# Performance work log

Measured on AMD Instinct MI355X. Metric: run time of the kernel, lower is better.

Reference implementation:

```python
import jax, jax.numpy as jnp
import numpy as np

KS = 3
ST = 1


def _windows(x, ks, st):
    """im2col sliding windows: (bs, c, h, w) -> (bs, c, H', W', ks, ks)
    where windows[b,c,i,j,k,f] = x[b,c, i*st+k, j*st+f] (matches torch as_strided)."""
    bs, c, h, w = x.shape
    Hp = (h - ks) // st + 1
    Wp = (w - ks) // st + 1
    return jnp.stack(
        [jnp.stack([x[:, :, k:k + Hp * st:st, f:f + Wp * st:st] for f in range(ks)], axis=-1)
         for k in range(ks)], axis=-2)


def setup_inputs() -> dict:
    key = jax.random.key(0)
    k1, k2, k3 = jax.random.split(key, 3)
    x = jax.random.normal(k1, (16, 16, 64, 512), dtype=jnp.float32)
    points = jax.random.normal(k2, (16, 3, 64, 512), dtype=jnp.float32)
    kernel = jax.random.normal(k3, (32, 16, 4), dtype=jnp.float32) * 0.05
    return {"x": x, "kernel": kernel, "points": points}


def reference(x, kernel, points):
    ks, st = KS, ST
    # (bs, in_c, H', W', ks, ks) overlapping patches of features and xyz coords
    strided_x = _windows(x, ks, st)
    strided_pts = _windows(points, ks, st)
    bd = ks // 2 if st == 1 else ks // 4
    # center point of each window: (bs, 3, H', W')
    ctr = points[:, :, bd:-bd, bd:-bd][:, :, ::st, ::st]
    # point-relative coordinates per window element: (bs, 3, H', W', ks, ks)
    rel_pts = ctr[..., None, None] - strided_pts
    # homogeneous coordinate -> d = 4
    rel_pts = jnp.concatenate([rel_pts, jnp.ones_like(rel_pts[:, :1])], axis=1)
    # kernel: (out_c, in_c, 4)
    return jnp.einsum('bdhwkf,bihwkf,oid->bohw', rel_pts, strided_x, kernel)
```

## Files before the change

kernel.cpp:

```cpp
#include <hip/hip_runtime.h>
#include <hip/hip_bf16.h>


#define HH 64
#define WW 512
#define HP 62
#define WP 510
#define IC 16
#define OC 32
#define BS 16
#define RB 2
#define TR (RB + 2)
#define TC 64
#define LC 68
#define NPL 19
#define CPR 17
#define NROWS (NPL * TR)
#define NCHUNK (NROWS * CPR)

typedef __attribute__((ext_vector_type(8))) short short8;
typedef __attribute__((ext_vector_type(4))) float f32x4;

static __device__ __forceinline__ short f2bf(float f) {
    union { __hip_bfloat16 h; short s; } u;
    u.h = __float2bfloat16(f);
    return u.s;
}

__global__ __launch_bounds__(256) void flex_conv_async(
    const float* __restrict__ x, const float* __restrict__ kern,
    const float* __restrict__ pts, float* __restrict__ out)
{
    __shared__ float lds[NPL * TR * LC];

    const int tid = threadIdx.x;
    const int j0 = blockIdx.x * TC;
    const int i0 = blockIdx.y * RB;
    const int b = blockIdx.z;

    const float* xb = x + (size_t)b * IC * HH * WW;
    const float* pb = pts + (size_t)b * 3 * HH * WW;

    #pragma unroll
    for (int rnd = 0; rnd < 6; ++rnd) {
        const int cid = tid + rnd * 256;
        if (cid < NCHUNK) {
            const int row = cid / CPR;
            const int chunk = cid - row * CPR;
            const int plane = row >> 2;
            const int rr = row & (TR - 1);
            const float* base = (plane < IC)
                ? (xb + (size_t)plane * HH * WW)
                : (pb + (size_t)(plane - IC) * HH * WW);
            int gcol = j0 + chunk * 4;
            if (gcol > WW - 4) gcol = WW - 4;
            const float* g = base + (size_t)(i0 + rr) * WW + gcol;
            __builtin_amdgcn_global_load_lds(
                (const __attribute__((address_space(1))) void*)g,
                (__attribute__((address_space(3))) void*)(lds + (size_t)cid * 4),
                16, 0, 0);
        }
    }

    const int lane = tid & 63;
    const int wave = tid >> 6;
    const int p = lane & 15;
    const int c = lane >> 4;
    const int tc = wave * 16 + p;

    short8 a0lo, a0hi, a1lo, a1hi;
    {
        const float4* k0v = (const float4*)(kern + (size_t)p * 64 + c * 8);
        const float4* k1v = (const float4*)(kern + (size_t)(16 + p) * 64 + c * 8);
        float4 v0a = k0v[0], v0b = k0v[1], v0c = k0v[8], v0d = k0v[9];
        float4 v1a = k1v[0], v1b = k1v[1], v1c = k1v[8], v1d = k1v[9];
        a0lo[0]=f2bf(v0a.x); a0lo[1]=f2bf(v0a.y); a0lo[2]=f2bf(v0a.z); a0lo[3]=f2bf(v0a.w);
        a0lo[4]=f2bf(v0b.x); a0lo[5]=f2bf(v0b.y); a0lo[6]=f2bf(v0b.z); a0lo[7]=f2bf(v0b.w);
        a0hi[0]=f2bf(v0c.x); a0hi[1]=f2bf(v0c.y); a0hi[2]=f2bf(v0c.z); a0hi[3]=f2bf(v0c.w);
        a0hi[4]=f2bf(v0d.x); a0hi[5]=f2bf(v0d.y); a0hi[6]=f2bf(v0d.z); a0hi[7]=f2bf(v0d.w);
        a1lo[0]=f2bf(v1a.x); a1lo[1]=f2bf(v1a.y); a1lo[2]=f2bf(v1a.z); a1lo[3]=f2bf(v1a.w);
        a1lo[4]=f2bf(v1b.x); a1lo[5]=f2bf(v1b.y); a1lo[6]=f2bf(v1b.z); a1lo[7]=f2bf(v1b.w);
        a1hi[0]=f2bf(v1c.x); a1hi[1]=f2bf(v1c.y); a1hi[2]=f2bf(v1c.z); a1hi[3]=f2bf(v1c.w);
        a1hi[4]=f2bf(v1d.x); a1hi[5]=f2bf(v1d.y); a1hi[6]=f2bf(v1d.z); a1hi[7]=f2bf(v1d.w);
    }

    __syncthreads();

    float xs[4][RB], px0[4][RB], px1[4][RB], px2[4][RB];
    #pragma unroll
    for (int t = 0; t < 4; ++t)
        #pragma unroll
        for (int q = 0; q < RB; ++q) { xs[t][q]=0.f; px0[t][q]=0.f; px1[t][q]=0.f; px2[t][q]=0.f; }
    float c0v[RB], c1v[RB], c2v[RB];

    #pragma unroll
    for (int rr = 0; rr < TR; ++rr) {
        const float* lp0 = &lds[(IC * TR + rr) * LC + tc];
        const float* lp1 = &lds[((IC + 1) * TR + rr) * LC + tc];
        const float* lp2 = &lds[((IC + 2) * TR + rr) * LC + tc];
        const float pa0 = lp0[0], pm0 = lp0[1], pz0 = lp0[2];
        const float pa1 = lp1[0], pm1 = lp1[1], pz1 = lp1[2];
        const float pa2 = lp2[0], pm2 = lp2[1], pz2 = lp2[2];
        if (rr >= 1 && rr <= RB) { c0v[rr-1] = pm0; c1v[rr-1] = pm1; c2v[rr-1] = pm2; }
        #pragma unroll
        for (int t = 0; t < 4; ++t) {
            const int ic = (t >> 1) * 8 + 2 * c + (t & 1);
            const float* lx = &lds[(ic * TR + rr) * LC + tc];
            const float x0 = lx[0], x1 = lx[1], x2 = lx[2];
            const float rsx = x0 + x1 + x2;
            float r0 = pa0 * x0; r0 = fmaf(pm0, x1, r0); r0 = fmaf(pz0, x2, r0);
            float r1 = pa1 * x0; r1 = fmaf(pm1, x1, r1); r1 = fmaf(pz1, x2, r1);
            float r2 = pa2 * x0; r2 = fmaf(pm2, x1, r2); r2 = fmaf(pz2, x2, r2);
            #pragma unroll
            for (int q = 0; q < RB; ++q) {
                if (rr >= q && rr <= q + 2) {
                    xs[t][q] += rsx; px0[t][q] += r0; px1[t][q] += r1; px2[t][q] += r2;
                }
            }
        }
    }

    const int j = j0 + tc;
    #pragma unroll
    for (int q = 0; q < RB; ++q) {
        short8 blo, bhi;
        #pragma unroll
        for (int t = 0; t < 4; ++t) {
            const short t0 = f2bf(fmaf(c0v[q], xs[t][q], -px0[t][q]));
            const short t1 = f2bf(fmaf(c1v[q], xs[t][q], -px1[t][q]));
            const short t2 = f2bf(fmaf(c2v[q], xs[t][q], -px2[t][q]));
            const short t3 = f2bf(xs[t][q]);
            const int s = (t & 1) * 4;
            if (t < 2) { blo[s+0]=t0; blo[s+1]=t1; blo[s+2]=t2; blo[s+3]=t3; }
            else       { bhi[s+0]=t0; bhi[s+1]=t1; bhi[s+2]=t2; bhi[s+3]=t3; }
        }
        f32x4 acc0 = {0.f,0.f,0.f,0.f}, acc1 = {0.f,0.f,0.f,0.f};
        acc0 = __builtin_amdgcn_mfma_f32_16x16x32_bf16(a0lo, blo, acc0, 0, 0, 0);
        acc0 = __builtin_amdgcn_mfma_f32_16x16x32_bf16(a0hi, bhi, acc0, 0, 0, 0);
        acc1 = __builtin_amdgcn_mfma_f32_16x16x32_bf16(a1lo, blo, acc1, 0, 0, 0);
        acc1 = __builtin_amdgcn_mfma_f32_16x16x32_bf16(a1hi, bhi, acc1, 0, 0, 0);
        if (j < WP) {
            float* ob = out + (size_t)b * OC * HP * WP + (size_t)(i0 + q) * WP + j;
            #pragma unroll
            for (int r = 0; r < 4; ++r) {
                const int o = c * 4 + r;
                ob[(size_t)o * HP * WP]        = acc0[r];
                ob[(size_t)(o + 16) * HP * WP] = acc1[r];
            }
        }
    }
}

extern "C" void kernel_launch(void* const* d_in, const int* in_sizes, int n_in,
                              void* d_out, int out_size, void* d_ws, size_t ws_size,
                              hipStream_t stream)
{
    const float* x    = (const float*)d_in[0];
    const float* kern = (const float*)d_in[1];
    const float* pts  = (const float*)d_in[2];
    float* out = (float*)d_out;

    dim3 block(256, 1, 1);
    dim3 grid(WW / TC, HP / RB, BS);
    flex_conv_async<<<grid, block, 0, stream>>>(x, kern, pts, out);
}
```

Measured before the change: 118.4 us.

## Double-buffer LDS tiles across a persistent row loop with taller row blocks

Each block now walks four consecutive row tiles and double-buffers the LDS staging. The next tile's global-to-LDS async loads are issued before computing the current one, so memory latency overlaps with compute. The row block grows from 2 to 4 output rows, which cuts the redundant halo rows loaded per output row. The cost is a much smaller grid (512 blocks instead of several thousand), about 62KB of LDS per block, and clamped duplicate work on the last tile. All of this can reduce occupancy and latency hiding.

After: 115.4 us. 2.6% less time.

```diff
diff --git a/kernel.cpp b/kernel.cpp
--- a/kernel.cpp
+++ b/kernel.cpp
@@ -9,7 +9,7 @@
 #define IC 16
 #define OC 32
 #define BS 16
-#define RB 2
+#define RB 4
 #define TR (RB + 2)
 #define TC 64
 #define LC 68
@@ -17,6 +17,9 @@
 #define CPR 17
 #define NROWS (NPL * TR)
 #define NCHUNK (NROWS * CPR)
+#define NRND 8
+#define TPG 4
+#define LDSZ (NPL * TR * LC)
 
 typedef __attribute__((ext_vector_type(8))) short short8;
 typedef __attribute__((ext_vector_type(4))) float f32x4;
@@ -27,38 +30,51 @@
     return u.s;
 }
 
-__global__ __launch_bounds__(256) void flex_conv_async(
+__global__ __launch_bounds__(256) void flex_conv_pipe(
     const float* __restrict__ x, const float* __restrict__ kern,
     const float* __restrict__ pts, float* __restrict__ out)
 {
-    __shared__ float lds[NPL * TR * LC];
+    __shared__ float lds[2][LDSZ];
 
     const int tid = threadIdx.x;
     const int j0 = blockIdx.x * TC;
-    const int i0 = blockIdx.y * RB;
-    const int b = blockIdx.z;
+    const int b  = blockIdx.z;
+    const int t0 = blockIdx.y * TPG;
 
     const float* xb = x + (size_t)b * IC * HH * WW;
     const float* pb = pts + (size_t)b * 3 * HH * WW;
 
+    const float* gbase[NRND];
+    bool act[NRND];
     #pragma unroll
-    for (int rnd = 0; rnd < 6; ++rnd) {
+    for (int rnd = 0; rnd < NRND; ++rnd) {
         const int cid = tid + rnd * 256;
-        if (cid < NCHUNK) {
-            const int row = cid / CPR;
-            const int chunk = cid - row * CPR;
-            const int plane = row >> 2;
-            const int rr = row & (TR - 1);
-            const float* base = (plane < IC)
-                ? (xb + (size_t)plane * HH * WW)
-                : (pb + (size_t)(plane - IC) * HH * WW);
-            int gcol = j0 + chunk * 4;
-            if (gcol > WW - 4) gcol = WW - 4;
-            const float* g = base + (size_t)(i0 + rr) * WW + gcol;
-            __builtin_amdgcn_global_load_lds(
-                (const __attribute__((address_space(1))) void*)g,
-                (__attribute__((address_space(3))) void*)(lds + (size_t)cid * 4),
-                16, 0, 0);
+        act[rnd] = (cid < NCHUNK);
+        const int cc = act[rnd] ? cid : 0;
+        const int row = cc / CPR;
+        const int chunk = cc - row * CPR;
+        const int plane = row / TR;
+        const int rr = row - plane * TR;
+        const float* base = (plane < IC)
+            ? (xb + (size_t)plane * HH * WW)
+            : (pb + (size_t)(plane - IC) * HH * WW);
+        int gcol = j0 + chunk * 4;
+        if (gcol > WW - 4) gcol = WW - 4;
+        gbase[rnd] = base + (size_t)rr * WW + gcol;
+    }
+
+    {
+        const int i00t = t0 * RB;
+        const int i00 = (i00t > HP - RB) ? (HP - RB) : i00t;
+        #pragma unroll
+        for (int rnd = 0; rnd < NRND; ++rnd) {
+            if (act[rnd]) {
+                const float* g = gbase[rnd] + (size_t)i00 * WW;
+                __builtin_amdgcn_global_load_lds(
+                    (const __attribute__((address_space(1))) void*)g,
+                    (__attribute__((address_space(3))) void*)(&lds[0][0] + (size_t)(tid + rnd * 256) * 4),
+                    16, 0, 0);
+            }
         }
     }
 
@@ -84,68 +100,91 @@
         a1hi[4]=f2bf(v1d.x); a1hi[5]=f2bf(v1d.y); a1hi[6]=f2bf(v1d.z); a1hi[7]=f2bf(v1d.w);
     }
 
-    __syncthreads();
-
-    float xs[4][RB], px0[4][RB], px1[4][RB], px2[4][RB];
-    #pragma unroll
-    for (int t = 0; t < 4; ++t)
-        #pragma unroll
-        for (int q = 0; q < RB; ++q) { xs[t][q]=0.f; px0[t][q]=0.f; px1[t][q]=0.f; px2[t][q]=0.f; }
-    float c0v[RB], c1v[RB], c2v[RB];
-
-    #pragma unroll
-    for (int rr = 0; rr < TR; ++rr) {
-        const float* lp0 = &lds[(IC * TR + rr) * LC + tc];
-        const float* lp1 = &lds[((IC + 1) * TR + rr) * LC + tc];
-        const float* lp2 = &lds[((IC + 2) * TR + rr) * LC + tc];
-        const float pa0 = lp0[0], pm0 = lp0[1], pz0 = lp0[2];
-        const float pa1 = lp1[0], pm1 = lp1[1], pz1 = lp1[2];
-        const float pa2 = lp2[0], pm2 = lp2[1], pz2 = lp2[2];
-        if (rr >= 1 && rr <= RB) { c0v[rr-1] = pm0; c1v[rr-1] = pm1; c2v[rr-1] = pm2; }
-        #pragma unroll
-        for (int t = 0; t < 4; ++t) {
-            const int ic = (t >> 1) * 8 + 2 * c + (t & 1);
-            const float* lx = &lds[(ic * TR + rr) * LC + tc];
-            const float x0 = lx[0], x1 = lx[1], x2 = lx[2];
-            const float rsx = x0 + x1 + x2;
-            float r0 = pa0 * x0; r0 = fmaf(pm0, x1, r0); r0 = fmaf(pz0, x2, r0);
-            float r1 = pa1 * x0; r1 = fmaf(pm1, x1, r1); r1 = fmaf(pz1, x2, r1);
-            float r2 = pa2 * x0; r2 = fmaf(pm2, x1, r2); r2 = fmaf(pz2, x2, r2);
-            #pragma unroll
-            for (int q = 0; q < RB; ++q) {
-                if (rr >= q && rr <= q + 2) {
-                    xs[t][q] += rsx; px0[t][q] += r0; px1[t][q] += r1; px2[t][q] += r2;
+    const int j = j0 + tc;
+
+    for (int s = 0; s < TPG; ++s) {
+        __syncthreads();
+
+        if (s + 1 < TPG) {
+            const int i1t = (t0 + s + 1) * RB;
+            const int i1 = (i1t > HP - RB) ? (HP - RB) : i1t;
+            float* dst = &lds[(s + 1) & 1][0];
+            #pragma unroll
+            for (int rnd = 0; rnd < NRND; ++rnd) {
+                if (act[rnd]) {
+                    const float* g = gbase[rnd] + (size_t)i1 * WW;
+                    __builtin_amdgcn_global_load_lds(
+                        (const __attribute__((address_space(1))) void*)g,
+                        (__attribute__((address_space(3))) void*)(dst + (size_t)(tid + rnd * 256) * 4),
+                        16, 0, 0);
                 }
             }
         }
-    }
-
-    const int j = j0 + tc;
-    #pragma unroll
-    for (int q = 0; q < RB; ++q) {
-        short8 blo, bhi;
-        #pragma unroll
-        for (int t = 0; t < 4; ++t) {
-            const short t0 = f2bf(fmaf(c0v[q], xs[t][q], -px0[t][q]));
-            const short t1 = f2bf(fmaf(c1v[q], xs[t][q], -px1[t][q]));
-            const short t2 = f2bf(fmaf(c2v[q], xs[t][q], -px2[t][q]));
-            const short t3 = f2bf(xs[t][q]);
-            const int s = (t & 1) * 4;
-            if (t < 2) { blo[s+0]=t0; blo[s+1]=t1; blo[s+2]=t2; blo[s+3]=t3; }
-            else       { bhi[s+0]=t0; bhi[s+1]=t1; bhi[s+2]=t2; bhi[s+3]=t3; }
-        }
-        f32x4 acc0 = {0.f,0.f,0.f,0.f}, acc1 = {0.f,0.f,0.f,0.f};
-        acc0 = __builtin_amdgcn_mfma_f32_16x16x32_bf16(a0lo, blo, acc0, 0, 0, 0);
-        acc0 = __builtin_amdgcn_mfma_f32_16x16x32_bf16(a0hi, bhi, acc0, 0, 0, 0);
-        acc1 = __builtin_amdgcn_mfma_f32_16x16x32_bf16(a1lo, blo, acc1, 0, 0, 0);
-        acc1 = __builtin_amdgcn_mfma_f32_16x16x32_bf16(a1hi, bhi, acc1, 0, 0, 0);
-        if (j < WP) {
-            float* ob = out + (size_t)b * OC * HP * WP + (size_t)(i0 + q) * WP + j;
-            #pragma unroll
-            for (int r = 0; r < 4; ++r) {
-                const int o = c * 4 + r;
-                ob[(size_t)o * HP * WP]        = acc0[r];
-                ob[(size_t)(o + 16) * HP * WP] = acc1[r];
+
+        const int i0t = (t0 + s) * RB;
+        const int i0 = (i0t > HP - RB) ? (HP - RB) : i0t;
+        const float* ldsb = &lds[s & 1][0];
+
+        float xs[4][RB], px0[4][RB], px1[4][RB], px2[4][RB];
+        #pragma unroll
+        for (int t = 0; t < 4; ++t)
+            #pragma unroll
+            for (int q = 0; q < RB; ++q) { xs[t][q]=0.f; px0[t][q]=0.f; px1[t][q]=0.f; px2[t][q]=0.f; }
+        float c0v[RB], c1v[RB], c2v[RB];
+
+        #pragma unroll
+        for (int rr = 0; rr < TR; ++rr) {
+            const float* lp0 = &ldsb[(IC * TR + rr) * LC + tc];
+            const float* lp1 = &ldsb[((IC + 1) * TR + rr) * LC + tc];
+            const float* lp2 = &ldsb[((IC + 2) * TR + rr) * LC + tc];
+            const float pa0 = lp0[0], pm0 = lp0[1], pz0 = lp0[2];
+            const float pa1 = lp1[0], pm1 = lp1[1], pz1 = lp1[2];
+            const float pa2 = lp2[0], pm2 = lp2[1], pz2 = lp2[2];
+            if (rr >= 1 && rr <= RB) { c0v[rr-1] = pm0; c1v[rr-1] = pm1; c2v[rr-1] = pm2; }
+            #pragma unroll
+            for (int t = 0; t < 4; ++t) {
+                const int ic = (t >> 1) * 8 + 2 * c + (t & 1);
+                const float* lx = &ldsb[(ic * TR + rr) * LC + tc];
+                const float x0 = lx[0], x1 = lx[1], x2 = lx[2];
+                const float rsx = x0 + x1 + x2;
+                float r0 = pa0 * x0; r0 = fmaf(pm0, x1, r0); r0 = fmaf(pz0, x2, r0);
+                float r1 = pa1 * x0; r1 = fmaf(pm1, x1, r1); r1 = fmaf(pz1, x2, r1);
+                float r2 = pa2 * x0; r2 = fmaf(pm2, x1, r2); r2 = fmaf(pz2, x2, r2);
+                #pragma unroll
+                for (int q = 0; q < RB; ++q) {
+                    if (rr >= q && rr <= q + 2) {
+                        xs[t][q] += rsx; px0[t][q] += r0; px1[t][q] += r1; px2[t][q] += r2;
+                    }
+                }
+            }
+        }
+
+        #pragma unroll
+        for (int q = 0; q < RB; ++q) {
+            short8 blo, bhi;
+            #pragma unroll
+            for (int t = 0; t < 4; ++t) {
+                const short e0 = f2bf(fmaf(c0v[q], xs[t][q], -px0[t][q]));
+                const short e1 = f2bf(fmaf(c1v[q], xs[t][q], -px1[t][q]));
+                const short e2 = f2bf(fmaf(c2v[q], xs[t][q], -px2[t][q]));
+                const short e3 = f2bf(xs[t][q]);
+                const int sl = (t & 1) * 4;
+                if (t < 2) { blo[sl+0]=e0; blo[sl+1]=e1; blo[sl+2]=e2; blo[sl+3]=e3; }
+                else       { bhi[sl+0]=e0; bhi[sl+1]=e1; bhi[sl+2]=e2; bhi[sl+3]=e3; }
+            }
+            f32x4 acc0 = {0.f,0.f,0.f,0.f}, acc1 = {0.f,0.f,0.f,0.f};
+            acc0 = __builtin_amdgcn_mfma_f32_16x16x32_bf16(a0lo, blo, acc0, 0, 0, 0);
+            acc0 = __builtin_amdgcn_mfma_f32_16x16x32_bf16(a0hi, bhi, acc0, 0, 0, 0);
+            acc1 = __builtin_amdgcn_mfma_f32_16x16x32_bf16(a1lo, blo, acc1, 0, 0, 0);
+            acc1 = __builtin_amdgcn_mfma_f32_16x16x32_bf16(a1hi, bhi, acc1, 0, 0, 0);
+            if (j < WP) {
+                float* ob = out + (size_t)b * OC * HP * WP + (size_t)(i0 + q) * WP + j;
+                #pragma unroll
+                for (int r = 0; r < 4; ++r) {
+                    const int o = c * 4 + r;
+                    ob[(size_t)o * HP * WP]        = acc0[r];
+                    ob[(size_t)(o + 16) * HP * WP] = acc1[r];
+                }
             }
         }
     }
@@ -161,6 +200,6 @@
     float* out = (float*)d_out;
 
     dim3 block(256, 1, 1);
-    dim3 grid(WW / TC, HP / RB, BS);
-    flex_conv_async<<<grid, block, 0, stream>>>(x, kern, pts, out);
+    dim3 grid(WW / TC, 4, BS);
+    flex_conv_pipe<<<grid, block, 0, stream>>>(x, kern, pts, out);
 }
```

## Give each wave a private LDS tile and replace block barrier with waitcnt

Applied to the files above, without the earlier changes.

Each wave now loads its own 16-column by 6-row halo tile for all 19 planes into a private LDS region and waits only on its own outstanding loads instead of a block-wide barrier. Each thread also computes 4 output rows instead of 2, with the last row-block clamped so it overlaps the previous one. This removes the block-level __syncthreads and raises per-thread work. In exchange, LDS traffic grows because halo columns are duplicated per wave, and the clamped last tile recomputes and rewrites some rows.

New measurement: 117.0 us. Within noise of the previous version (-1.2%).

```diff
diff --git a/kernel.cpp b/kernel.cpp
--- a/kernel.cpp
+++ b/kernel.cpp
@@ -9,14 +9,13 @@
 #define IC 16
 #define OC 32
 #define BS 16
-#define RB 2
-#define TR (RB + 2)
-#define TC 64
-#define LC 68
+#define RB 4
+#define TRW 6
+#define LCW 20
 #define NPL 19
-#define CPR 17
-#define NROWS (NPL * TR)
-#define NCHUNK (NROWS * CPR)
+#define WROWS (NPL * TRW)
+#define WCHUNK (WROWS * 5)
+#define WFLOATS (WCHUNK * 4)
 
 typedef __attribute__((ext_vector_type(8))) short short8;
 typedef __attribute__((ext_vector_type(4))) float f32x4;
@@ -27,46 +26,48 @@
     return u.s;
 }
 
-__global__ __launch_bounds__(256) void flex_conv_async(
+__global__ __launch_bounds__(256) void flex_conv_wave(
     const float* __restrict__ x, const float* __restrict__ kern,
     const float* __restrict__ pts, float* __restrict__ out)
 {
-    __shared__ float lds[NPL * TR * LC];
+    __shared__ float lds[4 * WFLOATS];
 
     const int tid = threadIdx.x;
-    const int j0 = blockIdx.x * TC;
-    const int i0 = blockIdx.y * RB;
+    const int lane = tid & 63;
+    const int wave = tid >> 6;
+    const int strip = blockIdx.x * 4 + wave;
+    const int j0 = strip * 16;
+    const int i0t = blockIdx.y * RB;
+    const int i0 = (i0t > HP - RB) ? (HP - RB) : i0t;
     const int b = blockIdx.z;
 
+    float* wlds = &lds[wave * WFLOATS];
     const float* xb = x + (size_t)b * IC * HH * WW;
     const float* pb = pts + (size_t)b * 3 * HH * WW;
 
     #pragma unroll
-    for (int rnd = 0; rnd < 6; ++rnd) {
-        const int cid = tid + rnd * 256;
-        if (cid < NCHUNK) {
-            const int row = cid / CPR;
-            const int chunk = cid - row * CPR;
-            const int plane = row >> 2;
-            const int rr = row & (TR - 1);
+    for (int r = 0; r < 9; ++r) {
+        const int cid = r * 64 + lane;
+        if (cid < WCHUNK) {
+            const int row = cid / 5;
+            const int ch = cid - row * 5;
+            const int plane = row / TRW;
+            const int rr = row - plane * TRW;
             const float* base = (plane < IC)
                 ? (xb + (size_t)plane * HH * WW)
                 : (pb + (size_t)(plane - IC) * HH * WW);
-            int gcol = j0 + chunk * 4;
+            int gcol = j0 + ch * 4;
             if (gcol > WW - 4) gcol = WW - 4;
             const float* g = base + (size_t)(i0 + rr) * WW + gcol;
             __builtin_amdgcn_global_load_lds(
                 (const __attribute__((address_space(1))) void*)g,
-                (__attribute__((address_space(3))) void*)(lds + (size_t)cid * 4),
+                (__attribute__((address_space(3))) void*)(wlds + (size_t)cid * 4),
                 16, 0, 0);
         }
     }
 
-    const int lane = tid & 63;
-    const int wave = tid >> 6;
     const int p = lane & 15;
     const int c = lane >> 4;
-    const int tc = wave * 16 + p;
 
     short8 a0lo, a0hi, a1lo, a1hi;
     {
@@ -84,7 +85,7 @@
         a1hi[4]=f2bf(v1d.x); a1hi[5]=f2bf(v1d.y); a1hi[6]=f2bf(v1d.z); a1hi[7]=f2bf(v1d.w);
     }
 
-    __syncthreads();
+    __builtin_amdgcn_s_waitcnt(0x0F70);
 
     float xs[4][RB], px0[4][RB], px1[4][RB], px2[4][RB];
     #pragma unroll
@@ -94,10 +95,10 @@
     float c0v[RB], c1v[RB], c2v[RB];
 
     #pragma unroll
-    for (int rr = 0; rr < TR; ++rr) {
-        const float* lp0 = &lds[(IC * TR + rr) * LC + tc];
-        const float* lp1 = &lds[((IC + 1) * TR + rr) * LC + tc];
-        const float* lp2 = &lds[((IC + 2) * TR + rr) * LC + tc];
+    for (int rr = 0; rr < TRW; ++rr) {
+        const float* lp0 = &wlds[(IC * TRW + rr) * LCW + p];
+        const float* lp1 = &wlds[((IC + 1) * TRW + rr) * LCW + p];
+        const float* lp2 = &wlds[((IC + 2) * TRW + rr) * LCW + p];
         const float pa0 = lp0[0], pm0 = lp0[1], pz0 = lp0[2];
         const float pa1 = lp1[0], pm1 = lp1[1], pz1 = lp1[2];
         const float pa2 = lp2[0], pm2 = lp2[1], pz2 = lp2[2];
@@ -105,7 +106,7 @@
         #pragma unroll
         for (int t = 0; t < 4; ++t) {
             const int ic = (t >> 1) * 8 + 2 * c + (t & 1);
-            const float* lx = &lds[(ic * TR + rr) * LC + tc];
+            const float* lx = &wlds[(ic * TRW + rr) * LCW + p];
             const float x0 = lx[0], x1 = lx[1], x2 = lx[2];
             const float rsx = x0 + x1 + x2;
             float r0 = pa0 * x0; r0 = fmaf(pm0, x1, r0); r0 = fmaf(pz0, x2, r0);
@@ -120,19 +121,19 @@
         }
     }
 
-    const int j = j0 + tc;
+    const int j = j0 + p;
     #pragma unroll
     for (int q = 0; q < RB; ++q) {
         short8 blo, bhi;
         #pragma unroll
         for (int t = 0; t < 4; ++t) {
-            const short t0 = f2bf(fmaf(c0v[q], xs[t][q], -px0[t][q]));
-            const short t1 = f2bf(fmaf(c1v[q], xs[t][q], -px1[t][q]));
-            const short t2 = f2bf(fmaf(c2v[q], xs[t][q], -px2[t][q]));
-            const short t3 = f2bf(xs[t][q]);
-            const int s = (t & 1) * 4;
-            if (t < 2) { blo[s+0]=t0; blo[s+1]=t1; blo[s+2]=t2; blo[s+3]=t3; }
-            else       { bhi[s+0]=t0; bhi[s+1]=t1; bhi[s+2]=t2; bhi[s+3]=t3; }
+            const short e0 = f2bf(fmaf(c0v[q], xs[t][q], -px0[t][q]));
+            const short e1 = f2bf(fmaf(c1v[q], xs[t][q], -px1[t][q]));
+            const short e2 = f2bf(fmaf(c2v[q], xs[t][q], -px2[t][q]));
+            const short e3 = f2bf(xs[t][q]);
+            const int sl = (t & 1) * 4;
+            if (t < 2) { blo[sl+0]=e0; blo[sl+1]=e1; blo[sl+2]=e2; blo[sl+3]=e3; }
+            else       { bhi[sl+0]=e0; bhi[sl+1]=e1; bhi[sl+2]=e2; bhi[sl+3]=e3; }
         }
         f32x4 acc0 = {0.f,0.f,0.f,0.f}, acc1 = {0.f,0.f,0.f,0.f};
         acc0 = __builtin_amdgcn_mfma_f32_16x16x32_bf16(a0lo, blo, acc0, 0, 0, 0);
@@ -161,6 +162,6 @@
     float* out = (float*)d_out;
 
     dim3 block(256, 1, 1);
-    dim3 grid(WW / TC, HP / RB, BS);
-    flex_conv_async<<<grid, block, 0, stream>>>(x, kern, pts, out);
+    dim3 grid(8, 16, BS);
+    flex_conv_wave<<<grid, block, 0, stream>>>(x, kern, pts, out);
 }
```
